# Kernel optimization log

Measured on AMD Instinct MI355X. Metric: run time of the kernel, lower is better.

## Reference

```python
import jax, jax.numpy as jnp
import numpy as np

NW, NT, ND, D = 30000, 2000, 20000, 128
E = {'ww': 600000, 'wt': 300000, 'wd': 400000, 'td': 100000, 'tt': 40000}
ENDS = {'ww': (NW, NW), 'wt': (NW, NT), 'wd': (NW, ND), 'td': (NT, ND), 'tt': (NT, NT)}


def setup_inputs() -> dict:
    key = jax.random.key(0)
    ks = iter(jax.random.split(key, 64))
    nrm = lambda shape: jax.random.normal(next(ks), shape, dtype=jnp.float32)
    inp = {}
    inp['feat_word'] = nrm((NW, D))
    inp['feat_topic'] = nrm((NT, D))
    # 'effect' node data: ~half the topics are causal (nonzero effect)
    inp['effect'] = jax.random.randint(next(ks), (NT,), 0, 2).astype(jnp.float32)
    # independent Bernoulli(0.1) draws for the td and tt iterations
    inp['bern_td'] = (jax.random.uniform(next(ks), (NT,)) < 0.1).astype(jnp.float32)
    inp['bern_tt'] = (jax.random.uniform(next(ks), (NT,)) < 0.1).astype(jnp.float32)
    for et, (ns, nd) in ENDS.items():
        inp[f'src_{et}'] = jax.random.randint(next(ks), (E[et],), 0, ns, dtype=jnp.int32)
        inp[f'dst_{et}'] = jax.random.randint(next(ks), (E[et],), 0, nd, dtype=jnp.int32)
        inp[f'w_{et}'] = jax.random.uniform(next(ks), (E[et],), dtype=jnp.float32)
    for name in ['ww', 'wt', 'wd', 'td', 'tt']:
        inp[f'W_{name}'] = nrm((D, D)) * 0.05
        inp[f'b_{name}'] = jnp.zeros((D,), jnp.float32)
    inp['W_causal'] = nrm((D, D)) * 0.05
    inp['W_noise'] = nrm((D, D)) * 0.05
    inp['n_doc'] = ND
    return inp


def _mean_agg(Wh, w, src, dst, n_dst):
    # DGL fn.u_mul_e + fn.mean: mean of (Wh[src]*w) over incoming edges; 0 for isolated dst
    m = Wh[src] * w[:, None]                                    # [E, D]
    s = jax.ops.segment_sum(m, dst, num_segments=n_dst)          # [n_dst, D]
    deg = jax.ops.segment_sum(jnp.ones_like(w), dst, num_segments=n_dst)
    return jnp.where(deg[:, None] > 0, s / jnp.maximum(deg, 1.0)[:, None], 0.0)


def reference(feat_word, feat_topic, effect, bern_td, bern_tt,
              src_ww, dst_ww, w_ww, src_wt, dst_wt, w_wt,
              src_wd, dst_wd, w_wd, src_td, dst_td, w_td,
              src_tt, dst_tt, w_tt,
              W_ww, b_ww, W_wt, b_wt, W_wd, b_wd, W_td, b_td, W_tt, b_tt,
              W_causal, W_noise, n_doc):
    n_word, n_topic = feat_word.shape[0], feat_topic.shape[0]
    # Phase 1: word -> word (ww)
    h_word = _mean_agg(feat_word @ W_ww + b_ww, w_ww, src_ww, dst_ww, n_word)
    # Phase 2: remaining etypes; word features replaced by h
    causal = (effect != 0).astype(feat_topic.dtype)[:, None]     # [NT, 1]
    rm_td = (bern_td * (effect == 0))[:, None]
    rm_tt = (bern_tt * (effect == 0))[:, None]
    Wh_wt = h_word @ W_wt + b_wt
    Wh_wd = h_word @ W_wd + b_wd
    Wh_td = (feat_topic @ W_td + b_td
             + (feat_topic * causal) @ W_causal - (feat_topic * rm_td) @ W_noise)
    Wh_tt = (feat_topic @ W_tt + b_tt
             + (feat_topic * causal) @ W_causal - (feat_topic * rm_tt) @ W_noise)
    # cross-relation 'sum' reducer per destination ntype
    h_topic = (_mean_agg(Wh_wt, w_wt, src_wt, dst_wt, n_topic)
               + _mean_agg(Wh_tt, w_tt, src_tt, dst_tt, n_topic))
    h_doc = (_mean_agg(Wh_wd, w_wd, src_wd, dst_wd, n_doc)
             + _mean_agg(Wh_td, w_td, src_td, dst_td, n_doc))
    return h_word, h_topic, h_doc
```

## Files before the change

kernel.cpp:

```cpp
#include <hip/hip_runtime.h>

#define D 128
typedef unsigned short u16;
constexpr int NW = 30000;
constexpr int NT = 2000;
constexpr int NDOC = 20000;

constexpr int CAPB = 1024;
constexpr int SSP  = 136;
constexpr int NBK_WW = (NW + 31) / 32;
constexpr int NBK_WT = NT / 4;
constexpr int NBK_TT = (NT + 31) / 32;
constexpr int NBK_WD = (NDOC + 31) / 32;
constexpr int NBK_TD = (NDOC + 31) / 32;
constexpr int BUK_WW = 0;
constexpr int BUK_WT = BUK_WW + NBK_WW;
constexpr int BUK_TT = BUK_WT + NBK_WT;
constexpr int BUK_WD = BUK_TT + NBK_TT;
constexpr int BUK_TD = BUK_WD + NBK_WD;
constexpr int NBUK   = BUK_TD + NBK_TD;

constexpr int EPB = 4096;
constexpr int NF2B = (NW * D / 4 + 255) / 256;
constexpr int NBM4 = (NT + 63) / 64;

struct RelDesc { const int* src; const int* dst; const float* w;
                 int e0; int buk0; int shift; int mask; };
struct Rels { RelDesc r[5]; };

__device__ __forceinline__ int which_rel(const Rels& R, int e)
{
    if (e < R.r[1].e0) return 0;
    if (e < R.r[2].e0) return 1;
    if (e < R.r[3].e0) return 2;
    if (e < R.r[4].e0) return 3;
    return 4;
}

__device__ __forceinline__ float b2f(u16 h)
{
    return __uint_as_float(((unsigned)h) << 16);
}
__device__ __forceinline__ u16 f2b(float f)
{
    unsigned u = __float_as_uint(f);
    return (u16)((u + 0x7FFF + ((u >> 16) & 1)) >> 16);
}

typedef short bf16x8 __attribute__((ext_vector_type(8)));
typedef float f32x4 __attribute__((ext_vector_type(4)));
constexpr int WPITCH = 136;

__device__ __forceinline__ void stage_wt(
    const float* __restrict__ Wg, u16* Wt, int tid)
{
    for (int i = tid; i < D * D; i += 256) {
        int k = i >> 7, nn = i & 127;
        Wt[nn * WPITCH + k] = f2b(Wg[i]);
    }
}

__device__ __forceinline__ void mfma_tile_f32(
    const float* __restrict__ X, const u16* Wt, int arow, int n,
    int lanelo, int quad, f32x4 acc[8])
{
#pragma unroll
    for (int ct = 0; ct < 8; ++ct) {
        acc[ct][0] = 0.f; acc[ct][1] = 0.f; acc[ct][2] = 0.f; acc[ct][3] = 0.f;
    }
#pragma unroll
    for (int k0 = 0; k0 < 4; ++k0) {
        bf16x8 a;
        if (arow < n) {
            const float* ap = X + (size_t)arow * D + k0 * 32 + quad * 8;
            float4 a0 = *(const float4*)ap;
            float4 a1 = *(const float4*)(ap + 4);
            a[0] = (short)f2b(a0.x); a[1] = (short)f2b(a0.y);
            a[2] = (short)f2b(a0.z); a[3] = (short)f2b(a0.w);
            a[4] = (short)f2b(a1.x); a[5] = (short)f2b(a1.y);
            a[6] = (short)f2b(a1.z); a[7] = (short)f2b(a1.w);
        } else {
#pragma unroll
            for (int j = 0; j < 8; ++j) a[j] = 0;
        }
#pragma unroll
        for (int ct = 0; ct < 8; ++ct) {
            bf16x8 b = *(const bf16x8*)&Wt[(ct * 16 + lanelo) * WPITCH
                                           + k0 * 32 + quad * 8];
            acc[ct] = __builtin_amdgcn_mfma_f32_16x16x32_bf16(a, b, acc[ct], 0, 0, 0);
        }
    }
}

struct MM4 { const float* W[4]; float* P[4]; };
struct TR3 { const float* W[3]; u16* T[3]; };

__global__ __launch_bounds__(256) void prep_kernel(
    const float* __restrict__ feat_word, u16* __restrict__ fw16,
    const float* __restrict__ feat_topic, MM4 m4, TR3 tr, int* __restrict__ cur)
{
    __shared__ u16 Wt[D * WPITCH];
    int tid = threadIdx.x;

    if ((int)blockIdx.x < NF2B) {
        int i = blockIdx.x * 256 + tid;
        if (i < NW * D / 4) {
            float4 v = ((const float4*)feat_word)[i];
            ushort4 o;
            o.x = f2b(v.x); o.y = f2b(v.y); o.z = f2b(v.z); o.w = f2b(v.w);
            ((ushort4*)fw16)[i] = o;
        }
    } else if ((int)blockIdx.x < NF2B + 4 * NBM4) {
        int idx = blockIdx.x - NF2B;
        int which = idx / NBM4;
        int bx = idx % NBM4;
        stage_wt(m4.W[which], Wt, tid);
        __syncthreads();
        int wv = tid >> 6, lane = tid & 63;
        int lanelo = lane & 15, quad = lane >> 4;
        int rowbase = bx * 64 + wv * 16;
        f32x4 acc[8];
        mfma_tile_f32(feat_topic, Wt, rowbase + lanelo, NT, lanelo, quad, acc);
        float* Y = m4.P[which];
        int rbase = rowbase + quad * 4;
#pragma unroll
        for (int r = 0; r < 4; ++r) {
            int row = rbase + r;
            if (row >= NT) continue;
#pragma unroll
            for (int ct = 0; ct < 8; ++ct)
                Y[(size_t)row * D + ct * 16 + lanelo] = acc[ct][r];
        }
    } else if ((int)blockIdx.x < NF2B + 4 * NBM4 + 3) {
        int which = blockIdx.x - NF2B - 4 * NBM4;
        stage_wt(tr.W[which], Wt, tid);
        __syncthreads();
        u16* Wd = tr.T[which];
        for (int i = tid; i < D * D; i += 256) {
            int nrow = i >> 7, k = i & 127;
            Wd[i] = Wt[nrow * WPITCH + k];
        }
    } else {
        for (int i = tid; i < NBUK; i += 256) cur[i] = 0;
    }
}

__global__ __launch_bounds__(256) void part_combine_kernel(
    Rels R, int Etot, int* __restrict__ cur, int2* __restrict__ edataP,
    const float* __restrict__ P_td, const float* __restrict__ P_tt,
    const float* __restrict__ Pc, const float* __restrict__ Pn,
    const float* __restrict__ effect, const float* __restrict__ bern_td,
    const float* __restrict__ bern_tt,
    const float* __restrict__ b_td, const float* __restrict__ b_tt,
    u16* __restrict__ wtd16, u16* __restrict__ wtt16, int npb)
{
    __shared__ int hist[NBUK];
    __shared__ int baseL[NBUK];
    int tid = threadIdx.x;

    if ((int)blockIdx.x >= npb) {
        int i = ((int)blockIdx.x - npb) * 256 + tid;
        if (i < NT * D) {
            int row = i >> 7;
            int col = i & (D - 1);
            float eff = effect[row];
            float causal = (eff != 0.f) ? 1.f : 0.f;
            float zero = (eff == 0.f) ? 1.f : 0.f;
            float rmtd = bern_td[row] * zero;
            float rmtt = bern_tt[row] * zero;
            float pc = Pc[i];
            float pn = Pn[i];
            wtd16[i] = f2b(P_td[i] + b_td[col] + causal * pc - rmtd * pn);
            wtt16[i] = f2b(P_tt[i] + b_tt[col] + causal * pc - rmtt * pn);
        }
        return;
    }

    for (int i = tid; i < NBUK; i += 256) hist[i] = 0;
    __syncthreads();
    int base_e = blockIdx.x * EPB;
    int bs[EPB / 256];
    int2 se[EPB / 256];
#pragma unroll
    for (int r = 0; r < EPB / 256; ++r) {
        int e = base_e + r * 256 + tid;
        if (e < Etot) {
            int k = which_rel(R, e);
            int le = e - R.r[k].e0;
            int s = R.r[k].src[le];
            int dd = R.r[k].dst[le];
            float w = R.r[k].w[le];
            int b = R.r[k].buk0 + (dd >> R.r[k].shift);
            int dloc = dd & R.r[k].mask;
            bs[r] = b;
            se[r] = make_int2(s | (dloc << 15), __float_as_int(w));
            atomicAdd(&hist[b], 1);
        } else {
            bs[r] = -1;
        }
    }
    __syncthreads();
    for (int i = tid; i < NBUK; i += 256)
        baseL[i] = hist[i] ? atomicAdd(&cur[i], hist[i]) : 0;
    __syncthreads();
    for (int i = tid; i < NBUK; i += 256) hist[i] = 0;
    __syncthreads();
#pragma unroll
    for (int r = 0; r < EPB / 256; ++r) {
        int b = bs[r];
        if (b >= 0) {
            int rk = atomicAdd(&hist[b], 1) + baseL[b];
            if (rk < CAPB)
                edataP[(size_t)b * CAPB + rk] = se[r];
        }
    }
}

struct BucketSmem {
    int2 st[CAPB];
    u16  Ssum[32 * SSP];
    float degL[32];
    float wsumL[32];
    int h2[32], exc[32], cnt[32];
};

__device__ __forceinline__ void reduce_one_lds(
    const u16* __restrict__ Xb, const int2* st,
    int start, int end, int dl, int lane, BucketSmem& s)
{
    int half = lane >> 5;
    int q = (lane & 31) * 4;
    float4 acc = make_float4(0.f, 0.f, 0.f, 0.f);
    float wacc = 0.f;
    int j = start;
    for (; j + 32 <= end; j += 32) {
        int2 ee[16];
        ushort4 vv[16];
#pragma unroll
        for (int t = 0; t < 16; ++t) ee[t] = st[j + 2 * t + half];
#pragma unroll
        for (int t = 0; t < 16; ++t)
            vv[t] = *(const ushort4*)(Xb + (size_t)(ee[t].x & 0x7FFF) * D + q);
#pragma unroll
        for (int t = 0; t < 16; ++t) {
            float w = __int_as_float(ee[t].y);
            acc.x = fmaf(w, b2f(vv[t].x), acc.x);
            acc.y = fmaf(w, b2f(vv[t].y), acc.y);
            acc.z = fmaf(w, b2f(vv[t].z), acc.z);
            acc.w = fmaf(w, b2f(vv[t].w), acc.w);
            wacc += w;
        }
    }
    if (j + 16 <= end) {
        int2 ee[8];
        ushort4 vv[8];
#pragma unroll
        for (int t = 0; t < 8; ++t) ee[t] = st[j + 2 * t + half];
#pragma unroll
        for (int t = 0; t < 8; ++t)
            vv[t] = *(const ushort4*)(Xb + (size_t)(ee[t].x & 0x7FFF) * D + q);
#pragma unroll
        for (int t = 0; t < 8; ++t) {
            float w = __int_as_float(ee[t].y);
            acc.x = fmaf(w, b2f(vv[t].x), acc.x);
            acc.y = fmaf(w, b2f(vv[t].y), acc.y);
            acc.z = fmaf(w, b2f(vv[t].z), acc.z);
            acc.w = fmaf(w, b2f(vv[t].w), acc.w);
            wacc += w;
        }
        j += 16;
    }
    if (j + 8 <= end) {
        int2 ee[4];
        ushort4 vv[4];
#pragma unroll
        for (int t = 0; t < 4; ++t) ee[t] = st[j + 2 * t + half];
#pragma unroll
        for (int t = 0; t < 4; ++t)
            vv[t] = *(const ushort4*)(Xb + (size_t)(ee[t].x & 0x7FFF) * D + q);
#pragma unroll
        for (int t = 0; t < 4; ++t) {
            float w = __int_as_float(ee[t].y);
            acc.x = fmaf(w, b2f(vv[t].x), acc.x);
            acc.y = fmaf(w, b2f(vv[t].y), acc.y);
            acc.z = fmaf(w, b2f(vv[t].z), acc.z);
            acc.w = fmaf(w, b2f(vv[t].w), acc.w);
            wacc += w;
        }
        j += 8;
    }
    if (j + 4 <= end) {
        int2 ea = st[j + half];
        int2 eb = st[j + 2 + half];
        ushort4 va = *(const ushort4*)(Xb + (size_t)(ea.x & 0x7FFF) * D + q);
        ushort4 vb = *(const ushort4*)(Xb + (size_t)(eb.x & 0x7FFF) * D + q);
        float wa = __int_as_float(ea.y);
        float wb = __int_as_float(eb.y);
        acc.x = fmaf(wa, b2f(va.x), acc.x); acc.y = fmaf(wa, b2f(va.y), acc.y);
        acc.z = fmaf(wa, b2f(va.z), acc.z); acc.w = fmaf(wa, b2f(va.w), acc.w);
        acc.x = fmaf(wb, b2f(vb.x), acc.x); acc.y = fmaf(wb, b2f(vb.y), acc.y);
        acc.z = fmaf(wb, b2f(vb.z), acc.z); acc.w = fmaf(wb, b2f(vb.w), acc.w);
        wacc += wa + wb;
        j += 4;
    }
    for (; j < end; j += 2) {
        int jj = j + half;
        int2 e = st[jj < end ? jj : (end - 1)];
        float w = (jj < end) ? __int_as_float(e.y) : 0.f;
        ushort4 v = *(const ushort4*)(Xb + (size_t)(e.x & 0x7FFF) * D + q);
        acc.x = fmaf(w, b2f(v.x), acc.x); acc.y = fmaf(w, b2f(v.y), acc.y);
        acc.z = fmaf(w, b2f(v.z), acc.z); acc.w = fmaf(w, b2f(v.w), acc.w);
        wacc += w;
    }
    acc.x += __shfl_xor(acc.x, 32);
    acc.y += __shfl_xor(acc.y, 32);
    acc.z += __shfl_xor(acc.z, 32);
    acc.w += __shfl_xor(acc.w, 32);
    wacc  += __shfl_xor(wacc, 32);
    if (half == 0) {
        ushort4 o;
        o.x = f2b(acc.x); o.y = f2b(acc.y); o.z = f2b(acc.z); o.w = f2b(acc.w);
        *(ushort4*)(s.Ssum + dl * SSP + q) = o;
    }
    if (lane == 0) {
        s.degL[dl] = (float)(end - start);
        s.wsumL[dl] = wacc;
    }
}

__device__ __forceinline__ void bucket_reduce(
    const u16* __restrict__ X, const int* __restrict__ cur,
    const int2* __restrict__ edataP, int buk, int nsl, BucketSmem& s)
{
    int tid = threadIdx.x;
    int nE = min(cur[buk], CAPB);
    const int2* gsrc = edataP + (size_t)buk * CAPB;
    int2 ev[CAPB / 256];
#pragma unroll
    for (int t = 0; t < CAPB / 256; ++t) {
        int i = t * 256 + tid;
        if (i < nE) ev[t] = gsrc[i];
    }
    if (tid < 32) { s.h2[tid] = 0; s.cnt[tid] = 0; }
    __syncthreads();
#pragma unroll
    for (int t = 0; t < CAPB / 256; ++t) {
        int i = t * 256 + tid;
        if (i < nE) atomicAdd(&s.h2[(ev[t].x >> 15) & 31], 1);
    }
    __syncthreads();
    if (tid < 32) s.exc[tid] = s.h2[tid];
    __syncthreads();
    for (int off = 1; off < 32; off <<= 1) {
        int t = 0;
        if (tid < 32 && tid >= off) t = s.exc[tid - off];
        __syncthreads();
        if (tid < 32) s.exc[tid] += t;
        __syncthreads();
    }
    if (tid < 32) s.exc[tid] -= s.h2[tid];
    __syncthreads();
#pragma unroll
    for (int t = 0; t < CAPB / 256; ++t) {
        int i = t * 256 + tid;
        if (i < nE) {
            int dl = (ev[t].x >> 15) & 31;
            int rk = atomicAdd(&s.cnt[dl], 1);
            s.st[s.exc[dl] + rk] = ev[t];
        }
    }
    __syncthreads();
    int wv = tid >> 6, lane = tid & 63;
    for (int dl = wv; dl < nsl; dl += 4) {
        int start = s.exc[dl];
        reduce_one_lds(X, s.st, start, start + s.h2[dl], dl, lane, s);
    }
}

__device__ __forceinline__ void fused_mm(
    BucketSmem& s, const u16* __restrict__ Wtg, const float* __restrict__ bias,
    const u16* __restrict__ Tg, const float* __restrict__ degTg,
    float* __restrict__ Y, u16* __restrict__ Yb, int row0, int n, int tid)
{
    int wv = tid >> 6, lane = tid & 63;
    int lanelo = lane & 15, quad = lane >> 4;
    int rt = wv >> 1, ch = wv & 1;
    int arow = rt * 16 + lanelo;
    f32x4 acc[4];
#pragma unroll
    for (int c = 0; c < 4; ++c) {
        acc[c][0] = 0.f; acc[c][1] = 0.f; acc[c][2] = 0.f; acc[c][3] = 0.f;
    }
#pragma unroll
    for (int k0 = 0; k0 < 4; ++k0) {
        bf16x8 a;
        if (arow < n) {
            a = *(const bf16x8*)(s.Ssum + arow * SSP + k0 * 32 + quad * 8);
        } else {
#pragma unroll
            for (int j = 0; j < 8; ++j) a[j] = 0;
        }
#pragma unroll
        for (int c = 0; c < 4; ++c) {
            int ct = ch * 4 + c;
            bf16x8 b = *(const bf16x8*)(Wtg + (ct * 16 + lanelo) * D
                                        + k0 * 32 + quad * 8);
            acc[c] = __builtin_amdgcn_mfma_f32_16x16x32_bf16(a, b, acc[c], 0, 0, 0);
        }
    }
    int rbase = rt * 16 + quad * 4;
#pragma unroll
    for (int r = 0; r < 4; ++r) {
        int row = rbase + r;
        if (row >= n) continue;
        float dgv = s.degL[row];
        float wsv = s.wsumL[row];
        float dtv = degTg ? degTg[row] : 0.f;
#pragma unroll
        for (int c = 0; c < 4; ++c) {
            int ct = ch * 4 + c;
            int col = ct * 16 + lanelo;
            float y = acc[c][r];
            y = dgv > 0.f ? (y + wsv * bias[col]) / dgv : 0.f;
            if (Tg && dtv > 0.f) y += b2f(Tg[(size_t)row * D + col]) / dtv;
            Y[(size_t)(row0 + row) * D + col] = y;
            if (Yb) Yb[(size_t)(row0 + row) * D + col] = f2b(y);
        }
    }
}

__device__ __forceinline__ void dump_smem(
    BucketSmem& s, u16* __restrict__ Sg, float* __restrict__ degg,
    int nsl, int tid)
{
    for (int i = tid; i < nsl * 32; i += 256) {
        int row = i >> 5, c4 = (i & 31) * 4;
        *(ushort4*)(Sg + (size_t)row * D + c4) =
            *(const ushort4*)(s.Ssum + row * SSP + c4);
    }
    if (tid < nsl) degg[tid] = s.degL[tid];
}

__global__ __launch_bounds__(256, 4) void phaseA_kernel(
    const u16* __restrict__ fw16, const u16* __restrict__ wtt16,
    const u16* __restrict__ wtd16, const int* __restrict__ cur,
    const int2* __restrict__ edataP,
    const u16* __restrict__ Wtg_ww, const float* __restrict__ b_ww,
    float* __restrict__ h_word, u16* __restrict__ hw16,
    u16* __restrict__ Sb2, float* __restrict__ degf2)
{
    __shared__ BucketSmem s;
    int b = blockIdx.x;
    int tid = threadIdx.x;
    if (b < NBK_WW) {
        int w0 = b * 32;
        int nsl = min(32, NW - w0);
        bucket_reduce(fw16, cur, edataP, BUK_WW + b, nsl, s);
        __syncthreads();
        fused_mm(s, Wtg_ww, b_ww, nullptr, nullptr, h_word, hw16, w0, nsl, tid);
    } else if (b < NBK_WW + NBK_TT) {
        int i = b - NBK_WW;
        int t0 = i * 32;
        int nsl = min(32, NT - t0);
        bucket_reduce(wtt16, cur, edataP, BUK_TT + i, nsl, s);
        __syncthreads();
        dump_smem(s, Sb2 + (size_t)t0 * D, degf2 + t0, nsl, tid);
    } else {
        int i = b - NBK_WW - NBK_TT;
        int d0 = i * 32;
        int nsl = min(32, NDOC - d0);
        bucket_reduce(wtd16, cur, edataP, BUK_TD + i, nsl, s);
        __syncthreads();
        dump_smem(s, Sb2 + (size_t)(NT + d0) * D, degf2 + NT + d0, nsl, tid);
    }
}

__global__ __launch_bounds__(256, 4) void phaseB_kernel(
    const u16* __restrict__ hw16, const int* __restrict__ cur,
    const int2* __restrict__ edataP,
    const u16* __restrict__ Wtg_wt, const float* __restrict__ b_wt,
    const u16* __restrict__ Wtg_wd, const float* __restrict__ b_wd,
    const u16* __restrict__ Sb2, const float* __restrict__ degf2,
    float* __restrict__ h_topic, float* __restrict__ h_doc)
{
    __shared__ BucketSmem s;
    int b = blockIdx.x;
    int tid = threadIdx.x;
    if (b < NBK_WT) {
        int t0 = b * 4;
        bucket_reduce(hw16, cur, edataP, BUK_WT + b, 4, s);
        __syncthreads();
        fused_mm(s, Wtg_wt, b_wt, Sb2 + (size_t)t0 * D, degf2 + t0,
                 h_topic, nullptr, t0, 4, tid);
    } else {
        int i = b - NBK_WT;
        int d0 = i * 32;
        int nsl = min(32, NDOC - d0);
        bucket_reduce(hw16, cur, edataP, BUK_WD + i, nsl, s);
        __syncthreads();
        fused_mm(s, Wtg_wd, b_wd, Sb2 + (size_t)(NT + d0) * D, degf2 + NT + d0,
                 h_doc, nullptr, d0, nsl, tid);
    }
}

extern "C" void kernel_launch(void* const* d_in, const int* in_sizes, int n_in,
                              void* d_out, int out_size, void* d_ws, size_t ws_size,
                              hipStream_t stream)
{
    const float* feat_word  = (const float*)d_in[0];
    const float* feat_topic = (const float*)d_in[1];
    const float* effect     = (const float*)d_in[2];
    const float* bern_td    = (const float*)d_in[3];
    const float* bern_tt    = (const float*)d_in[4];
    const int*   src_ww = (const int*)d_in[5];
    const int*   dst_ww = (const int*)d_in[6];
    const float* w_ww   = (const float*)d_in[7];
    const int*   src_wt = (const int*)d_in[8];
    const int*   dst_wt = (const int*)d_in[9];
    const float* w_wt   = (const float*)d_in[10];
    const int*   src_wd = (const int*)d_in[11];
    const int*   dst_wd = (const int*)d_in[12];
    const float* w_wd   = (const float*)d_in[13];
    const int*   src_td = (const int*)d_in[14];
    const int*   dst_td = (const int*)d_in[15];
    const float* w_td   = (const float*)d_in[16];
    const int*   src_tt = (const int*)d_in[17];
    const int*   dst_tt = (const int*)d_in[18];
    const float* w_tt   = (const float*)d_in[19];
    const float* W_ww = (const float*)d_in[20];
    const float* b_ww = (const float*)d_in[21];
    const float* W_wt = (const float*)d_in[22];
    const float* b_wt = (const float*)d_in[23];
    const float* W_wd = (const float*)d_in[24];
    const float* b_wd = (const float*)d_in[25];
    const float* W_td = (const float*)d_in[26];
    const float* b_td = (const float*)d_in[27];
    const float* W_tt = (const float*)d_in[28];
    const float* b_tt = (const float*)d_in[29];
    const float* W_causal = (const float*)d_in[30];
    const float* W_noise  = (const float*)d_in[31];

    const int E_ww = in_sizes[5];
    const int E_wt = in_sizes[8];
    const int E_wd = in_sizes[11];
    const int E_td = in_sizes[14];
    const int E_tt = in_sizes[17];
    const int E_total = E_ww + E_wt + E_wd + E_td + E_tt;

    float* ws = (float*)d_ws;
    u16*   Sb2   = (u16*)ws; ws += (long long)(NT + NDOC) * D / 2;
    float* degf2 = ws; ws += NT + NDOC;
    int*   cur   = (int*)ws; ws += NBUK;
    ws += ((size_t)(ws - (float*)d_ws) & 1);
    int2*  edataP = (int2*)ws; ws += (long long)2 * NBUK * CAPB;
    float* P_td  = ws; ws += (long long)NT * D;
    float* P_tt  = ws; ws += (long long)NT * D;
    float* Pc    = ws; ws += (long long)NT * D;
    float* Pn    = ws; ws += (long long)NT * D;
    u16*   fw16  = (u16*)ws;  ws += (long long)NW * D / 2;
    u16*   hw16  = (u16*)ws;  ws += (long long)NW * D / 2;
    u16*   wtd16 = (u16*)ws;  ws += (long long)NT * D / 2;
    u16*   wtt16 = (u16*)ws;  ws += (long long)NT * D / 2;
    u16*   Wtg_ww = (u16*)ws; ws += (long long)D * D / 2;
    u16*   Wtg_wt = (u16*)ws; ws += (long long)D * D / 2;
    u16*   Wtg_wd = (u16*)ws; ws += (long long)D * D / 2;

    float* h_word  = (float*)d_out;
    float* h_topic = h_word + (long long)NW * D;
    float* h_doc   = h_topic + (long long)NT * D;

    auto nb = [](long long n) { return (unsigned)((n + 255) / 256); };

    Rels R;
    R.r[0] = { src_ww, dst_ww, w_ww, 0,                         BUK_WW, 5, 31 };
    R.r[1] = { src_wt, dst_wt, w_wt, E_ww,                      BUK_WT, 2, 3  };
    R.r[2] = { src_tt, dst_tt, w_tt, E_ww + E_wt,               BUK_TT, 5, 31 };
    R.r[3] = { src_wd, dst_wd, w_wd, E_ww + E_wt + E_tt,        BUK_WD, 5, 31 };
    R.r[4] = { src_td, dst_td, w_td, E_ww + E_wt + E_tt + E_wd, BUK_TD, 5, 31 };

    MM4 m4;
    m4.W[0] = W_td; m4.W[1] = W_tt; m4.W[2] = W_causal; m4.W[3] = W_noise;
    m4.P[0] = P_td; m4.P[1] = P_tt; m4.P[2] = Pc;       m4.P[3] = Pn;
    TR3 tr;
    tr.W[0] = W_ww; tr.W[1] = W_wt; tr.W[2] = W_wd;
    tr.T[0] = Wtg_ww; tr.T[1] = Wtg_wt; tr.T[2] = Wtg_wd;
    prep_kernel<<<NF2B + 4 * NBM4 + 3 + 1, 256, 0, stream>>>(
        feat_word, fw16, feat_topic, m4, tr, cur);

    unsigned npb = (unsigned)((E_total + EPB - 1) / EPB);
    part_combine_kernel<<<npb + nb((long long)NT * D), 256, 0, stream>>>(
        R, E_total, cur, edataP,
        P_td, P_tt, Pc, Pn, effect, bern_td, bern_tt, b_td, b_tt,
        wtd16, wtt16, (int)npb);

    phaseA_kernel<<<NBK_WW + NBK_TT + NBK_TD, 256, 0, stream>>>(
        fw16, wtt16, wtd16, cur, edataP, Wtg_ww, b_ww,
        h_word, hw16, Sb2, degf2);

    phaseB_kernel<<<NBK_WT + NBK_WD, 256, 0, stream>>>(
        hw16, cur, edataP, Wtg_wt, b_wt, Wtg_wd, b_wd,
        Sb2, degf2, h_topic, h_doc);

    (void)n_in; (void)in_sizes; (void)out_size; (void)ws_size;
}
```

Baseline: 251.8 us.

## Fuse four phase kernels into one cooperative persistent kernel with grid syncs

Merges the prep, partition/combine, phase A and phase B kernels into a single cooperative kernel. Each phase's work units are distributed over a persistent grid capped at 1024 blocks, and the phases are separated by grid.sync, with the four-launch path kept as a fallback. The aim is to remove the launch gaps and tail drain between kernels. In exchange it adds grid-wide barrier cost, shares one union of shared memory across phases (which may lower occupancy), and runs each phase with fewer blocks than units, so blocks loop over several units.

```diff
diff --git a/kernel.cpp b/kernel.cpp
--- a/kernel.cpp
+++ b/kernel.cpp
@@ -1,4 +1,6 @@
 #include <hip/hip_runtime.h>
+#include <hip/hip_cooperative_groups.h>
+namespace cg = cooperative_groups;
 
 #define D 128
 typedef unsigned short u16;
@@ -20,9 +22,15 @@
 constexpr int BUK_TD = BUK_WD + NBK_WD;
 constexpr int NBUK   = BUK_TD + NBK_TD;
 
-constexpr int EPB = 4096;
+constexpr int EPB  = 4096;
 constexpr int NF2B = (NW * D / 4 + 255) / 256;
 constexpr int NBM4 = (NT + 63) / 64;
+constexpr int NZU  = (NBUK + 255) / 256;
+constexpr int NCMB = (NT * D + 255) / 256;
+constexpr int U1 = NF2B + 4 * NBM4 + 3 + NZU;
+constexpr int U3 = NBK_WW + NBK_TT + NBK_TD;
+constexpr int U4 = NBK_WT + NBK_WD;
+constexpr int MAXGRID = 1024;
 
 struct RelDesc { const int* src; const int* dst; const float* w;
                  int e0; int buk0; int shift; int mask; };
@@ -50,6 +58,37 @@
 typedef short bf16x8 __attribute__((ext_vector_type(8)));
 typedef float f32x4 __attribute__((ext_vector_type(4)));
 constexpr int WPITCH = 136;
+
+struct BucketSmem {
+    int2 st[CAPB];
+    u16  Ssum[32 * SSP];
+    float degL[32];
+    float wsumL[32];
+    int h2[32], exc[32], cnt[32];
+};
+struct PartSm { int hist[NBUK]; int baseL[NBUK]; };
+union Smem {
+    u16 Wt[D * WPITCH];
+    BucketSmem bs;
+    PartSm pt;
+};
+
+struct MM4 { const float* W[4]; float* P[4]; };
+
+struct FP {
+    const float *feat_word, *feat_topic;
+    const float *effect, *bern_td, *bern_tt;
+    Rels R;
+    int Etot, npb;
+    MM4 m4;
+    const float *W_ww, *W_wt, *W_wd;
+    const float *b_ww, *b_wt, *b_wd, *b_td, *b_tt;
+    int* cur; int2* edataP;
+    u16 *fw16, *hw16, *wtd16, *wtt16;
+    u16 *Wtg_ww, *Wtg_wt, *Wtg_wd;
+    u16* Sb2; float* degf2;
+    float *h_word, *h_topic, *h_doc;
+};
 
 __device__ __forceinline__ void stage_wt(
     const float* __restrict__ Wg, u16* Wt, int tid)
@@ -91,138 +130,6 @@
         }
     }
 }
-
-struct MM4 { const float* W[4]; float* P[4]; };
-struct TR3 { const float* W[3]; u16* T[3]; };
-
-__global__ __launch_bounds__(256) void prep_kernel(
-    const float* __restrict__ feat_word, u16* __restrict__ fw16,
-    const float* __restrict__ feat_topic, MM4 m4, TR3 tr, int* __restrict__ cur)
-{
-    __shared__ u16 Wt[D * WPITCH];
-    int tid = threadIdx.x;
-
-    if ((int)blockIdx.x < NF2B) {
-        int i = blockIdx.x * 256 + tid;
-        if (i < NW * D / 4) {
-            float4 v = ((const float4*)feat_word)[i];
-            ushort4 o;
-            o.x = f2b(v.x); o.y = f2b(v.y); o.z = f2b(v.z); o.w = f2b(v.w);
-            ((ushort4*)fw16)[i] = o;
-        }
-    } else if ((int)blockIdx.x < NF2B + 4 * NBM4) {
-        int idx = blockIdx.x - NF2B;
-        int which = idx / NBM4;
-        int bx = idx % NBM4;
-        stage_wt(m4.W[which], Wt, tid);
-        __syncthreads();
-        int wv = tid >> 6, lane = tid & 63;
-        int lanelo = lane & 15, quad = lane >> 4;
-        int rowbase = bx * 64 + wv * 16;
-        f32x4 acc[8];
-        mfma_tile_f32(feat_topic, Wt, rowbase + lanelo, NT, lanelo, quad, acc);
-        float* Y = m4.P[which];
-        int rbase = rowbase + quad * 4;
-#pragma unroll
-        for (int r = 0; r < 4; ++r) {
-            int row = rbase + r;
-            if (row >= NT) continue;
-#pragma unroll
-            for (int ct = 0; ct < 8; ++ct)
-                Y[(size_t)row * D + ct * 16 + lanelo] = acc[ct][r];
-        }
-    } else if ((int)blockIdx.x < NF2B + 4 * NBM4 + 3) {
-        int which = blockIdx.x - NF2B - 4 * NBM4;
-        stage_wt(tr.W[which], Wt, tid);
-        __syncthreads();
-        u16* Wd = tr.T[which];
-        for (int i = tid; i < D * D; i += 256) {
-            int nrow = i >> 7, k = i & 127;
-            Wd[i] = Wt[nrow * WPITCH + k];
-        }
-    } else {
-        for (int i = tid; i < NBUK; i += 256) cur[i] = 0;
-    }
-}
-
-__global__ __launch_bounds__(256) void part_combine_kernel(
-    Rels R, int Etot, int* __restrict__ cur, int2* __restrict__ edataP,
-    const float* __restrict__ P_td, const float* __restrict__ P_tt,
-    const float* __restrict__ Pc, const float* __restrict__ Pn,
-    const float* __restrict__ effect, const float* __restrict__ bern_td,
-    const float* __restrict__ bern_tt,
-    const float* __restrict__ b_td, const float* __restrict__ b_tt,
-    u16* __restrict__ wtd16, u16* __restrict__ wtt16, int npb)
-{
-    __shared__ int hist[NBUK];
-    __shared__ int baseL[NBUK];
-    int tid = threadIdx.x;
-
-    if ((int)blockIdx.x >= npb) {
-        int i = ((int)blockIdx.x - npb) * 256 + tid;
-        if (i < NT * D) {
-            int row = i >> 7;
-            int col = i & (D - 1);
-            float eff = effect[row];
-            float causal = (eff != 0.f) ? 1.f : 0.f;
-            float zero = (eff == 0.f) ? 1.f : 0.f;
-            float rmtd = bern_td[row] * zero;
-            float rmtt = bern_tt[row] * zero;
-            float pc = Pc[i];
-            float pn = Pn[i];
-            wtd16[i] = f2b(P_td[i] + b_td[col] + causal * pc - rmtd * pn);
-            wtt16[i] = f2b(P_tt[i] + b_tt[col] + causal * pc - rmtt * pn);
-        }
-        return;
-    }
-
-    for (int i = tid; i < NBUK; i += 256) hist[i] = 0;
-    __syncthreads();
-    int base_e = blockIdx.x * EPB;
-    int bs[EPB / 256];
-    int2 se[EPB / 256];
-#pragma unroll
-    for (int r = 0; r < EPB / 256; ++r) {
-        int e = base_e + r * 256 + tid;
-        if (e < Etot) {
-            int k = which_rel(R, e);
-            int le = e - R.r[k].e0;
-            int s = R.r[k].src[le];
-            int dd = R.r[k].dst[le];
-            float w = R.r[k].w[le];
-            int b = R.r[k].buk0 + (dd >> R.r[k].shift);
-            int dloc = dd & R.r[k].mask;
-            bs[r] = b;
-            se[r] = make_int2(s | (dloc << 15), __float_as_int(w));
-            atomicAdd(&hist[b], 1);
-        } else {
-            bs[r] = -1;
-        }
-    }
-    __syncthreads();
-    for (int i = tid; i < NBUK; i += 256)
-        baseL[i] = hist[i] ? atomicAdd(&cur[i], hist[i]) : 0;
-    __syncthreads();
-    for (int i = tid; i < NBUK; i += 256) hist[i] = 0;
-    __syncthreads();
-#pragma unroll
-    for (int r = 0; r < EPB / 256; ++r) {
-        int b = bs[r];
-        if (b >= 0) {
-            int rk = atomicAdd(&hist[b], 1) + baseL[b];
-            if (rk < CAPB)
-                edataP[(size_t)b * CAPB + rk] = se[r];
-        }
-    }
-}
-
-struct BucketSmem {
-    int2 st[CAPB];
-    u16  Ssum[32 * SSP];
-    float degL[32];
-    float wsumL[32];
-    int h2[32], exc[32], cnt[32];
-};
 
 __device__ __forceinline__ void reduce_one_lds(
     const u16* __restrict__ Xb, const int2* st,
@@ -441,66 +348,210 @@
     if (tid < nsl) degg[tid] = s.degL[tid];
 }
 
-__global__ __launch_bounds__(256, 4) void phaseA_kernel(
-    const u16* __restrict__ fw16, const u16* __restrict__ wtt16,
-    const u16* __restrict__ wtd16, const int* __restrict__ cur,
-    const int2* __restrict__ edataP,
-    const u16* __restrict__ Wtg_ww, const float* __restrict__ b_ww,
-    float* __restrict__ h_word, u16* __restrict__ hw16,
-    u16* __restrict__ Sb2, float* __restrict__ degf2)
-{
-    __shared__ BucketSmem s;
-    int b = blockIdx.x;
-    int tid = threadIdx.x;
-    if (b < NBK_WW) {
-        int w0 = b * 32;
+__device__ __forceinline__ void p1_unit(const FP& p, int u, u16* Wt, int tid)
+{
+    if (u < NF2B) {
+        int i = u * 256 + tid;
+        if (i < NW * D / 4) {
+            float4 v = ((const float4*)p.feat_word)[i];
+            ushort4 o;
+            o.x = f2b(v.x); o.y = f2b(v.y); o.z = f2b(v.z); o.w = f2b(v.w);
+            ((ushort4*)p.fw16)[i] = o;
+        }
+    } else if (u < NF2B + 4 * NBM4) {
+        int idx = u - NF2B;
+        int which = idx / NBM4;
+        int bx = idx % NBM4;
+        stage_wt(p.m4.W[which], Wt, tid);
+        __syncthreads();
+        int wv = tid >> 6, lane = tid & 63;
+        int lanelo = lane & 15, quad = lane >> 4;
+        int rowbase = bx * 64 + wv * 16;
+        f32x4 acc[8];
+        mfma_tile_f32(p.feat_topic, Wt, rowbase + lanelo, NT, lanelo, quad, acc);
+        float* Y = p.m4.P[which];
+        int rbase = rowbase + quad * 4;
+#pragma unroll
+        for (int r = 0; r < 4; ++r) {
+            int row = rbase + r;
+            if (row >= NT) continue;
+#pragma unroll
+            for (int ct = 0; ct < 8; ++ct)
+                Y[(size_t)row * D + ct * 16 + lanelo] = acc[ct][r];
+        }
+        __syncthreads();
+    } else if (u < NF2B + 4 * NBM4 + 3) {
+        int which = u - NF2B - 4 * NBM4;
+        const float* Wg = which == 0 ? p.W_ww : which == 1 ? p.W_wt : p.W_wd;
+        u16* Wd = which == 0 ? p.Wtg_ww : which == 1 ? p.Wtg_wt : p.Wtg_wd;
+        stage_wt(Wg, Wt, tid);
+        __syncthreads();
+        for (int i = tid; i < D * D; i += 256) {
+            int nrow = i >> 7, k = i & 127;
+            Wd[i] = Wt[nrow * WPITCH + k];
+        }
+        __syncthreads();
+    } else {
+        int i = (u - NF2B - 4 * NBM4 - 3) * 256 + tid;
+        if (i < NBUK) p.cur[i] = 0;
+    }
+}
+
+__device__ __forceinline__ void p2_unit(const FP& p, int u, PartSm& pt, int tid)
+{
+    if (u < p.npb) {
+        for (int i = tid; i < NBUK; i += 256) pt.hist[i] = 0;
+        __syncthreads();
+        int base_e = u * EPB;
+        int bs[EPB / 256];
+        int2 se[EPB / 256];
+#pragma unroll
+        for (int r = 0; r < EPB / 256; ++r) {
+            int e = base_e + r * 256 + tid;
+            if (e < p.Etot) {
+                int k = which_rel(p.R, e);
+                int le = e - p.R.r[k].e0;
+                int s = p.R.r[k].src[le];
+                int dd = p.R.r[k].dst[le];
+                float w = p.R.r[k].w[le];
+                int b = p.R.r[k].buk0 + (dd >> p.R.r[k].shift);
+                int dloc = dd & p.R.r[k].mask;
+                bs[r] = b;
+                se[r] = make_int2(s | (dloc << 15), __float_as_int(w));
+                atomicAdd(&pt.hist[b], 1);
+            } else {
+                bs[r] = -1;
+            }
+        }
+        __syncthreads();
+        for (int i = tid; i < NBUK; i += 256)
+            pt.baseL[i] = pt.hist[i] ? atomicAdd(&p.cur[i], pt.hist[i]) : 0;
+        __syncthreads();
+        for (int i = tid; i < NBUK; i += 256) pt.hist[i] = 0;
+        __syncthreads();
+#pragma unroll
+        for (int r = 0; r < EPB / 256; ++r) {
+            int b = bs[r];
+            if (b >= 0) {
+                int rk = atomicAdd(&pt.hist[b], 1) + pt.baseL[b];
+                if (rk < CAPB)
+                    p.edataP[(size_t)b * CAPB + rk] = se[r];
+            }
+        }
+        __syncthreads();
+    } else {
+        int i = (u - p.npb) * 256 + tid;
+        if (i < NT * D) {
+            int row = i >> 7;
+            int col = i & (D - 1);
+            float eff = p.effect[row];
+            float causal = (eff != 0.f) ? 1.f : 0.f;
+            float zero = (eff == 0.f) ? 1.f : 0.f;
+            float rmtd = p.bern_td[row] * zero;
+            float rmtt = p.bern_tt[row] * zero;
+            float pc = p.m4.P[2][i];
+            float pn = p.m4.P[3][i];
+            p.wtd16[i] = f2b(p.m4.P[0][i] + p.b_td[col] + causal * pc - rmtd * pn);
+            p.wtt16[i] = f2b(p.m4.P[1][i] + p.b_tt[col] + causal * pc - rmtt * pn);
+        }
+    }
+}
+
+__device__ __forceinline__ void p3_unit(const FP& p, int u, BucketSmem& bs, int tid)
+{
+    if (u < NBK_WW) {
+        int w0 = u * 32;
         int nsl = min(32, NW - w0);
-        bucket_reduce(fw16, cur, edataP, BUK_WW + b, nsl, s);
-        __syncthreads();
-        fused_mm(s, Wtg_ww, b_ww, nullptr, nullptr, h_word, hw16, w0, nsl, tid);
-    } else if (b < NBK_WW + NBK_TT) {
-        int i = b - NBK_WW;
+        bucket_reduce(p.fw16, p.cur, p.edataP, BUK_WW + u, nsl, bs);
+        __syncthreads();
+        fused_mm(bs, p.Wtg_ww, p.b_ww, nullptr, nullptr,
+                 p.h_word, p.hw16, w0, nsl, tid);
+        __syncthreads();
+    } else if (u < NBK_WW + NBK_TT) {
+        int i = u - NBK_WW;
         int t0 = i * 32;
         int nsl = min(32, NT - t0);
-        bucket_reduce(wtt16, cur, edataP, BUK_TT + i, nsl, s);
-        __syncthreads();
-        dump_smem(s, Sb2 + (size_t)t0 * D, degf2 + t0, nsl, tid);
+        bucket_reduce(p.wtt16, p.cur, p.edataP, BUK_TT + i, nsl, bs);
+        __syncthreads();
+        dump_smem(bs, p.Sb2 + (size_t)t0 * D, p.degf2 + t0, nsl, tid);
+        __syncthreads();
     } else {
-        int i = b - NBK_WW - NBK_TT;
+        int i = u - NBK_WW - NBK_TT;
         int d0 = i * 32;
         int nsl = min(32, NDOC - d0);
-        bucket_reduce(wtd16, cur, edataP, BUK_TD + i, nsl, s);
-        __syncthreads();
-        dump_smem(s, Sb2 + (size_t)(NT + d0) * D, degf2 + NT + d0, nsl, tid);
-    }
-}
-
-__global__ __launch_bounds__(256, 4) void phaseB_kernel(
-    const u16* __restrict__ hw16, const int* __restrict__ cur,
-    const int2* __restrict__ edataP,
-    const u16* __restrict__ Wtg_wt, const float* __restrict__ b_wt,
-    const u16* __restrict__ Wtg_wd, const float* __restrict__ b_wd,
-    const u16* __restrict__ Sb2, const float* __restrict__ degf2,
-    float* __restrict__ h_topic, float* __restrict__ h_doc)
-{
-    __shared__ BucketSmem s;
-    int b = blockIdx.x;
-    int tid = threadIdx.x;
-    if (b < NBK_WT) {
-        int t0 = b * 4;
-        bucket_reduce(hw16, cur, edataP, BUK_WT + b, 4, s);
-        __syncthreads();
-        fused_mm(s, Wtg_wt, b_wt, Sb2 + (size_t)t0 * D, degf2 + t0,
-                 h_topic, nullptr, t0, 4, tid);
+        bucket_reduce(p.wtd16, p.cur, p.edataP, BUK_TD + i, nsl, bs);
+        __syncthreads();
+        dump_smem(bs, p.Sb2 + (size_t)(NT + d0) * D, p.degf2 + NT + d0, nsl, tid);
+        __syncthreads();
+    }
+}
+
+__device__ __forceinline__ void p4_unit(const FP& p, int u, BucketSmem& bs, int tid)
+{
+    if (u < NBK_WT) {
+        int t0 = u * 4;
+        bucket_reduce(p.hw16, p.cur, p.edataP, BUK_WT + u, 4, bs);
+        __syncthreads();
+        fused_mm(bs, p.Wtg_wt, p.b_wt, p.Sb2 + (size_t)t0 * D,
+                 p.degf2 + t0, p.h_topic, nullptr, t0, 4, tid);
+        __syncthreads();
     } else {
-        int i = b - NBK_WT;
+        int i = u - NBK_WT;
         int d0 = i * 32;
         int nsl = min(32, NDOC - d0);
-        bucket_reduce(hw16, cur, edataP, BUK_WD + i, nsl, s);
-        __syncthreads();
-        fused_mm(s, Wtg_wd, b_wd, Sb2 + (size_t)(NT + d0) * D, degf2 + NT + d0,
-                 h_doc, nullptr, d0, nsl, tid);
-    }
+        bucket_reduce(p.hw16, p.cur, p.edataP, BUK_WD + i, nsl, bs);
+        __syncthreads();
+        fused_mm(bs, p.Wtg_wd, p.b_wd, p.Sb2 + (size_t)(NT + d0) * D,
+                 p.degf2 + NT + d0, p.h_doc, nullptr, d0, nsl, tid);
+        __syncthreads();
+    }
+}
+
+__global__ __launch_bounds__(256, 4) void fused_kernel(FP p)
+{
+    __shared__ Smem sm;
+    cg::grid_group grid = cg::this_grid();
+    int tid = threadIdx.x;
+    const int nb = (int)gridDim.x;
+
+    for (int u = blockIdx.x; u < U1; u += nb) p1_unit(p, u, sm.Wt, tid);
+    __threadfence();
+    grid.sync();
+
+    const int U2 = p.npb + NCMB;
+    for (int u = blockIdx.x; u < U2; u += nb) p2_unit(p, u, sm.pt, tid);
+    __threadfence();
+    grid.sync();
+
+    for (int u = blockIdx.x; u < U3; u += nb) p3_unit(p, u, sm.bs, tid);
+    __threadfence();
+    grid.sync();
+
+    for (int u = blockIdx.x; u < U4; u += nb) p4_unit(p, u, sm.bs, tid);
+}
+
+__global__ __launch_bounds__(256) void prep_kernel(FP p)
+{
+    __shared__ u16 Wt[D * WPITCH];
+    p1_unit(p, (int)blockIdx.x, Wt, threadIdx.x);
+}
+
+__global__ __launch_bounds__(256) void part_combine_kernel(FP p)
+{
+    __shared__ PartSm pt;
+    p2_unit(p, (int)blockIdx.x, pt, threadIdx.x);
+}
+
+__global__ __launch_bounds__(256, 4) void phaseA_kernel(FP p)
+{
+    __shared__ BucketSmem bs;
+    p3_unit(p, (int)blockIdx.x, bs, threadIdx.x);
+}
+
+__global__ __launch_bounds__(256, 4) void phaseB_kernel(FP p)
+{
+    __shared__ BucketSmem bs;
+    p4_unit(p, (int)blockIdx.x, bs, threadIdx.x);
 }
 
 extern "C" void kernel_launch(void* const* d_in, const int* in_sizes, int n_in,
@@ -569,37 +620,52 @@
     float* h_topic = h_word + (long long)NW * D;
     float* h_doc   = h_topic + (long long)NT * D;
 
-    auto nb = [](long long n) { return (unsigned)((n + 255) / 256); };
-
-    Rels R;
-    R.r[0] = { src_ww, dst_ww, w_ww, 0,                         BUK_WW, 5, 31 };
-    R.r[1] = { src_wt, dst_wt, w_wt, E_ww,                      BUK_WT, 2, 3  };
-    R.r[2] = { src_tt, dst_tt, w_tt, E_ww + E_wt,               BUK_TT, 5, 31 };
-    R.r[3] = { src_wd, dst_wd, w_wd, E_ww + E_wt + E_tt,        BUK_WD, 5, 31 };
-    R.r[4] = { src_td, dst_td, w_td, E_ww + E_wt + E_tt + E_wd, BUK_TD, 5, 31 };
-
-    MM4 m4;
-    m4.W[0] = W_td; m4.W[1] = W_tt; m4.W[2] = W_causal; m4.W[3] = W_noise;
-    m4.P[0] = P_td; m4.P[1] = P_tt; m4.P[2] = Pc;       m4.P[3] = Pn;
-    TR3 tr;
-    tr.W[0] = W_ww; tr.W[1] = W_wt; tr.W[2] = W_wd;
-    tr.T[0] = Wtg_ww; tr.T[1] = Wtg_wt; tr.T[2] = Wtg_wd;
-    prep_kernel<<<NF2B + 4 * NBM4 + 3 + 1, 256, 0, stream>>>(
-        feat_word, fw16, feat_topic, m4, tr, cur);
-
-    unsigned npb = (unsigned)((E_total + EPB - 1) / EPB);
-    part_combine_kernel<<<npb + nb((long long)NT * D), 256, 0, stream>>>(
-        R, E_total, cur, edataP,
-        P_td, P_tt, Pc, Pn, effect, bern_td, bern_tt, b_td, b_tt,
-        wtd16, wtt16, (int)npb);
-
-    phaseA_kernel<<<NBK_WW + NBK_TT + NBK_TD, 256, 0, stream>>>(
-        fw16, wtt16, wtd16, cur, edataP, Wtg_ww, b_ww,
-        h_word, hw16, Sb2, degf2);
-
-    phaseB_kernel<<<NBK_WT + NBK_WD, 256, 0, stream>>>(
-        hw16, cur, edataP, Wtg_wt, b_wt, Wtg_wd, b_wd,
-        Sb2, degf2, h_topic, h_doc);
+    FP p;
+    p.feat_word = feat_word; p.feat_topic = feat_topic;
+    p.effect = effect; p.bern_td = bern_td; p.bern_tt = bern_tt;
+    p.R.r[0] = { src_ww, dst_ww, w_ww, 0,                         BUK_WW, 5, 31 };
+    p.R.r[1] = { src_wt, dst_wt, w_wt, E_ww,                      BUK_WT, 2, 3  };
+    p.R.r[2] = { src_tt, dst_tt, w_tt, E_ww + E_wt,               BUK_TT, 5, 31 };
+    p.R.r[3] = { src_wd, dst_wd, w_wd, E_ww + E_wt + E_tt,        BUK_WD, 5, 31 };
+    p.R.r[4] = { src_td, dst_td, w_td, E_ww + E_wt + E_tt + E_wd, BUK_TD, 5, 31 };
+    p.Etot = E_total;
+    p.npb = (E_total + EPB - 1) / EPB;
+    p.m4.W[0] = W_td; p.m4.W[1] = W_tt; p.m4.W[2] = W_causal; p.m4.W[3] = W_noise;
+    p.m4.P[0] = P_td; p.m4.P[1] = P_tt; p.m4.P[2] = Pc;       p.m4.P[3] = Pn;
+    p.W_ww = W_ww; p.W_wt = W_wt; p.W_wd = W_wd;
+    p.b_ww = b_ww; p.b_wt = b_wt; p.b_wd = b_wd; p.b_td = b_td; p.b_tt = b_tt;
+    p.cur = cur; p.edataP = edataP;
+    p.fw16 = fw16; p.hw16 = hw16; p.wtd16 = wtd16; p.wtt16 = wtt16;
+    p.Wtg_ww = Wtg_ww; p.Wtg_wt = Wtg_wt; p.Wtg_wd = Wtg_wd;
+    p.Sb2 = Sb2; p.degf2 = degf2;
+    p.h_word = h_word; p.h_topic = h_topic; p.h_doc = h_doc;
+
+    bool coop_ok = false;
+    int nbpc = 0;
+    hipError_t oe = hipOccupancyMaxActiveBlocksPerMultiprocessor(
+        &nbpc, reinterpret_cast<const void*>(fused_kernel), 256, 0);
+    if (oe == hipSuccess && nbpc > 0) {
+        int ncu = 256;
+        int dev = 0;
+        if (hipGetDevice(&dev) == hipSuccess)
+            (void)hipDeviceGetAttribute(&ncu,
+                hipDeviceAttributeMultiprocessorCount, dev);
+        long long cap = (long long)nbpc * ncu;
+        unsigned grid = (unsigned)(cap < MAXGRID ? cap : MAXGRID);
+        if (grid >= 64) {
+            void* args[] = { (void*)&p };
+            hipError_t le = hipLaunchCooperativeKernel(
+                (const void*)fused_kernel, dim3(grid), dim3(256), args, 0, stream);
+            coop_ok = (le == hipSuccess);
+        }
+    }
+    if (!coop_ok) {
+        (void)hipGetLastError();
+        prep_kernel<<<U1, 256, 0, stream>>>(p);
+        part_combine_kernel<<<(unsigned)(p.npb + NCMB), 256, 0, stream>>>(p);
+        phaseA_kernel<<<U3, 256, 0, stream>>>(p);
+        phaseB_kernel<<<U4, 256, 0, stream>>>(p);
+    }
 
     (void)n_in; (void)in_sizes; (void)out_size; (void)ws_size;
 }
```

After: 706.1 us. 180% more time.
